# Kernel tuning notes

Measured on AMD Instinct MI355X. Metric: run time of the kernel, lower is better.

The kernel has to match this reference:

```python
import jax, jax.numpy as jnp
import numpy as np

N = 100000   # nodes
E = 1600000  # random edges per augmented graph (before self-loops)
F = 128      # input_dim
H = 128      # hidden_dim
K = 3        # n_clusters
L = 3        # num_layers


def setup_inputs() -> dict:
    key = jax.random.key(0)
    ks = jax.random.split(key, 24)
    x1 = jax.random.normal(ks[0], (N, F), jnp.float32)
    x2 = jax.random.normal(ks[1], (N, F), jnp.float32)
    x3 = jax.random.normal(ks[2], (N, F), jnp.float32)
    loops = jnp.arange(N, dtype=jnp.int32)
    self_loops = jnp.stack([loops, loops])  # [2, N]

    def aug_edges(k):
        e = jax.random.randint(k, (2, E), 0, N, dtype=jnp.int32)
        return jnp.concatenate([e, self_loops], axis=1)  # [2, E+N]

    e1 = aug_edges(ks[3])
    e2 = aug_edges(ks[4])
    e3 = aug_edges(ks[5])

    s = 1.0 / np.sqrt(H)
    Ws = jax.random.normal(ks[6], (L, H, H), jnp.float32) * s  # F == H
    bs = jnp.zeros((L, H), jnp.float32)
    a = jnp.float32(0.25)  # PReLU slope (torch default)
    cw1 = jax.random.normal(ks[7], (H, H), jnp.float32) * s
    cb1 = jnp.zeros((H,), jnp.float32)
    cw2 = jax.random.normal(ks[8], (H, K), jnp.float32) * s
    cb2 = jnp.zeros((K,), jnp.float32)
    iw1 = jax.random.normal(ks[9], (H, H), jnp.float32) * s
    ib1 = jnp.zeros((H,), jnp.float32)
    iw2 = jax.random.normal(ks[10], (H, H), jnp.float32) * s
    ib2 = jnp.zeros((H,), jnp.float32)
    return dict(x1=x1, x2=x2, x3=x3, e1=e1, e2=e2, e3=e3,
                Ws=Ws, bs=bs, a=a, cw1=cw1, cb1=cb1, cw2=cw2, cb2=cb2,
                iw1=iw1, ib1=ib1, iw2=iw2, ib2=ib2)


def _l2norm(z):
    # F.normalize(z, dim=1), eps=1e-12
    return z / jnp.maximum(jnp.linalg.norm(z, axis=1, keepdims=True), 1e-12)


def _gconv(x, edges, Ws, bs, a):
    # DGL GraphConv norm='left': messages from src scaled by 1/out_deg(src),
    # summed at dst, then linear + shared PReLU per layer; final row L2-norm.
    src, dst = edges[0], edges[1]
    deg = jax.ops.segment_sum(jnp.ones(src.shape[0], x.dtype), src, num_segments=N)
    inv = 1.0 / jnp.maximum(deg, 1.0)  # DGL clamps zero out-degree
    z = x
    for l in range(L):
        msg = (z * inv[:, None])[src]               # [E, H] gather
        agg = jax.ops.segment_sum(msg, dst, num_segments=N)  # [N, H] scatter-add
        z = agg @ Ws[l] + bs[l]
        z = jnp.where(z >= 0, z, a * z)             # PReLU
    return _l2norm(z)


def reference(x1, x2, x3, e1, e2, e3, Ws, bs, a,
              cw1, cb1, cw2, cb2, iw1, ib1, iw2, ib2):
    z1 = _gconv(x1, e1, Ws, bs, a)
    z2 = _gconv(x2, e2, Ws, bs, a)
    z3 = _gconv(x3, e3, Ws, bs, a)

    def cluster(z):
        h = jax.nn.elu(z @ cw1 + cb1)
        p = jax.nn.softmax(h @ cw2 + cb2, axis=1)
        return _l2norm(p)

    def inst(z):
        return jax.nn.elu(z @ iw1 + ib1) @ iw2 + ib2

    return (z3, inst(z1), inst(z2), cluster(z1), cluster(z2))
```

## Files before the change

kernel.cpp:

```cpp
#include <hip/hip_runtime.h>
#include <hip/hip_bf16.h>
#include <cmath>


typedef __attribute__((ext_vector_type(8))) short short8;
typedef __attribute__((ext_vector_type(4))) float floatx4;

#define NB_MAX 512
#define PART_B 256
#define LCSR_MAX 6144

static __device__ __forceinline__ unsigned short f2bf(float f) {
  unsigned u = __builtin_bit_cast(unsigned, f);
  u += 0x7fffu + ((u >> 16) & 1u);
  return (unsigned short)(u >> 16);
}
static __device__ __forceinline__ float bf2f(unsigned short h) {
  unsigned u = ((unsigned)h) << 16;
  return __builtin_bit_cast(float, u);
}
static __device__ __forceinline__ float bflo(unsigned v) {
  return __builtin_bit_cast(float, v << 16);
}
static __device__ __forceinline__ float bfhi(unsigned v) {
  return __builtin_bit_cast(float, v & 0xffff0000u);
}

static __device__ __forceinline__ floatx4 mfma16(short8 a, short8 b, floatx4 c) {
  return __builtin_amdgcn_mfma_f32_16x16x32_bf16(a, b, c, 0, 0, 0);
}

static __device__ __forceinline__ void mfma_block(
    const short8 a_h[2], const unsigned short* __restrict__ Wth,
    const unsigned short* __restrict__ Wtl, int ks, int lr, int lg,
    floatx4 acc[2][8]) {
#pragma unroll
  for (int nf = 0; nf < 8; ++nf) {
    size_t boff = (size_t)(nf * 16 + lr) * 128 + ks * 32 + lg * 8;
    short8 b_h = *(const short8*)(Wth + boff);
    short8 b_l = *(const short8*)(Wtl + boff);
#pragma unroll
    for (int mf = 0; mf < 2; ++mf) {
      acc[mf][nf] = mfma16(a_h[mf], b_h, acc[mf][nf]);
      acc[mf][nf] = mfma16(a_h[mf], b_l, acc[mf][nf]);
    }
  }
}


__global__ __launch_bounds__(256) void bucket_count(const int* __restrict__ src,
                                                    const int* __restrict__ dst,
                                                    int ne, int nb, int chunk,
                                                    int* __restrict__ bcnt,
                                                    int* __restrict__ deg) {
  __shared__ int h[NB_MAX];
  const int t = threadIdx.x, b = blockIdx.x;
  for (int i = t; i < nb; i += 256) h[i] = 0;
  __syncthreads();
  const int start = b * chunk, endi = min(start + chunk, ne);
  for (int i = start + t; i < endi; i += 256) {
    atomicAdd(&h[dst[i] >> 8], 1);
    atomicAdd(&deg[src[i]], 1);
  }
  __syncthreads();
  for (int i = t; i < nb; i += 256) bcnt[i * PART_B + b] = h[i];
}

__global__ __launch_bounds__(256) void partition_edges(
    const int* __restrict__ src, const int* __restrict__ dst, int ne, int nb,
    int chunk, const int* __restrict__ boff, int* __restrict__ part) {
  __shared__ int h[NB_MAX];
  const int t = threadIdx.x, b = blockIdx.x;
  for (int i = t; i < nb; i += 256) h[i] = boff[i * PART_B + b];
  __syncthreads();
  const int start = b * chunk, endi = min(start + chunk, ne);
  for (int i = start + t; i < endi; i += 256) {
    int d = dst[i];
    int gpos = atomicAdd(&h[d >> 8], 1);
    part[gpos] = (src[i] << 8) | (d & 255);
  }
}

__global__ __launch_bounds__(256) void fine_csr(const int* __restrict__ part,
                                                const int* __restrict__ boff,
                                                int nb, int n, int ne,
                                                int* __restrict__ row_ptr,
                                                int* __restrict__ csr) {
  __shared__ int s[256];
  __shared__ int cur[256];
  __shared__ int lcsr[LCSR_MAX];
  const int t = threadIdx.x, b2 = blockIdx.x;
  const int base = boff[b2 * PART_B];
  const int endb = boff[(b2 + 1) * PART_B];
  const int cnt_local = endb - base;
  const int node_base = b2 << 8;

  s[t] = 0;
  __syncthreads();
  for (int i = base + t; i < endb; i += 256) atomicAdd(&s[part[i] & 255], 1);
  __syncthreads();
  for (int d = 1; d < 256; d <<= 1) {
    int v = s[t];
    int a = (t >= d) ? s[t - d] : 0;
    __syncthreads();
    s[t] = v + a;
    __syncthreads();
  }
  int excl = (t == 0) ? 0 : s[t - 1];
  int node = node_base + t;
  if (node <= n) row_ptr[node] = base + excl;
  if (b2 == nb - 1 && t == 0) row_ptr[n] = ne;
  cur[t] = excl;
  __syncthreads();

  if (cnt_local <= LCSR_MAX) {
    for (int i = base + t; i < endb; i += 256) {
      int v = part[i];
      int p = atomicAdd(&cur[v & 255], 1);
      lcsr[p] = v >> 8;
    }
    __syncthreads();
    for (int i = t; i < cnt_local; i += 256) csr[base + i] = lcsr[i];
  } else {
    for (int i = base + t; i < endb; i += 256) {
      int v = part[i];
      int p = atomicAdd(&cur[v & 255], 1);
      csr[base + p] = v >> 8;
    }
  }
}

__global__ __launch_bounds__(256) void make_inv(const int* __restrict__ deg,
                                                float* __restrict__ inv, int n) {
  int i = blockIdx.x * blockDim.x + threadIdx.x;
  if (i < n) inv[i] = 1.0f / (float)(deg[i] + 1);
}

#define SCAN_B 256
#define SCAN_T 256

__global__ __launch_bounds__(SCAN_T) void scan_part(const int* __restrict__ cnt,
                                                    int n, int cpt,
                                                    int* __restrict__ partials) {
  __shared__ int red[SCAN_T];
  const int t = threadIdx.x, b = blockIdx.x;
  const int g = b * SCAN_T + t;
  const int start = g * cpt, endi = min(start + cpt, n);
  int s = 0;
  for (int i = start; i < endi; ++i) s += cnt[i];
  red[t] = s;
  __syncthreads();
  for (int d = SCAN_T / 2; d > 0; d >>= 1) {
    if (t < d) red[t] += red[t + d];
    __syncthreads();
  }
  if (t == 0) partials[b] = red[0];
}

__global__ __launch_bounds__(SCAN_B) void scan_offsets(
    const int* __restrict__ partials, int* __restrict__ block_off,
    int* __restrict__ row_ptr, int n) {
  __shared__ int sums[SCAN_B];
  const int t = threadIdx.x;
  sums[t] = partials[t];
  __syncthreads();
  for (int d = 1; d < SCAN_B; d <<= 1) {
    int v = sums[t];
    int a = (t >= d) ? sums[t - d] : 0;
    __syncthreads();
    sums[t] = v + a;
    __syncthreads();
  }
  block_off[t] = (t == 0) ? 0 : sums[t - 1];
  if (t == SCAN_B - 1) row_ptr[n] = sums[t];
}

__global__ __launch_bounds__(SCAN_T) void scan_fill(const int* __restrict__ cnt,
                                                    int n, int cpt,
                                                    const int* __restrict__ block_off,
                                                    int* __restrict__ row_ptr) {
  __shared__ int sums[SCAN_T];
  const int t = threadIdx.x, b = blockIdx.x;
  const int g = b * SCAN_T + t;
  const int start = g * cpt, endi = min(start + cpt, n);
  int s = 0;
  for (int i = start; i < endi; ++i) s += cnt[i];
  sums[t] = s;
  __syncthreads();
  for (int d = 1; d < SCAN_T; d <<= 1) {
    int v = sums[t];
    int a = (t >= d) ? sums[t - d] : 0;
    __syncthreads();
    sums[t] = v + a;
    __syncthreads();
  }
  int off = block_off[b] + ((t == 0) ? 0 : sums[t - 1]);
  for (int i = start; i < endi; ++i) {
    row_ptr[i] = off;
    off += cnt[i];
  }
}


__global__ __launch_bounds__(256) void scale_cast(const float* __restrict__ x,
                                                  const float* __restrict__ inv,
                                                  unsigned short* __restrict__ zsc,
                                                  int n) {
  int idx = blockIdx.x * blockDim.x + threadIdx.x;
  if (idx >= n * 32) return;
  int row = idx >> 5;
  float s = inv[row];
  float4 v = *(const float4*)(x + (size_t)idx * 4);
  unsigned u0 = (unsigned)f2bf(v.x * s) | ((unsigned)f2bf(v.y * s) << 16);
  unsigned u1 = (unsigned)f2bf(v.z * s) | ((unsigned)f2bf(v.w * s) << 16);
  uint2 p = {u0, u1};
  *(uint2*)(zsc + (size_t)idx * 4) = p;
}

__global__ __launch_bounds__(256) void prep_w(const float* __restrict__ src,
                                              unsigned short* __restrict__ dh,
                                              unsigned short* __restrict__ dl) {
  int idx = blockIdx.x * 256 + threadIdx.x;
  int k = idx >> 7, nn = idx & 127;
  float w = src[idx];
  unsigned short h = f2bf(w);
  dh[nn * 128 + k] = h;
  dl[nn * 128 + k] = f2bf(w - bf2f(h));
}


__global__ __launch_bounds__(256) void aggregate_bf16(
    const unsigned short* __restrict__ zsc, const int* __restrict__ row_ptr,
    const int* __restrict__ csr_src, unsigned short* __restrict__ ah, int n) {
  int w = (blockIdx.x * blockDim.x + threadIdx.x) >> 6;
  const int lane = threadIdx.x & 63;
  if (w >= n) return;
  w = __builtin_amdgcn_readfirstlane(w);
  const int beg = row_ptr[w], end = row_ptr[w + 1];
  const unsigned* zp = (const unsigned*)zsc;
  unsigned vs = zp[(size_t)w * 64 + lane];
  float ax0 = bflo(vs), ay0 = bfhi(vs), ax1 = 0.f, ay1 = 0.f;
  float ax2 = 0.f, ay2 = 0.f, ax3 = 0.f, ay3 = 0.f;
  for (int base = beg; base < end; base += 64) {
    const int cnt = min(64, end - base);
    int my = (base + lane < end) ? csr_src[base + lane] : 0;
    int e = 0;
    for (; e + 8 <= cnt; e += 8) {
      int s0 = __shfl(my, e);
      int s1 = __shfl(my, e + 1);
      int s2 = __shfl(my, e + 2);
      int s3 = __shfl(my, e + 3);
      int s4 = __shfl(my, e + 4);
      int s5 = __shfl(my, e + 5);
      int s6 = __shfl(my, e + 6);
      int s7 = __shfl(my, e + 7);
      unsigned v0 = zp[(size_t)s0 * 64 + lane];
      unsigned v1 = zp[(size_t)s1 * 64 + lane];
      unsigned v2 = zp[(size_t)s2 * 64 + lane];
      unsigned v3 = zp[(size_t)s3 * 64 + lane];
      unsigned v4 = zp[(size_t)s4 * 64 + lane];
      unsigned v5 = zp[(size_t)s5 * 64 + lane];
      unsigned v6 = zp[(size_t)s6 * 64 + lane];
      unsigned v7 = zp[(size_t)s7 * 64 + lane];
      ax0 += bflo(v0); ay0 += bfhi(v0);
      ax1 += bflo(v1); ay1 += bfhi(v1);
      ax2 += bflo(v2); ay2 += bfhi(v2);
      ax3 += bflo(v3); ay3 += bfhi(v3);
      ax0 += bflo(v4); ay0 += bfhi(v4);
      ax1 += bflo(v5); ay1 += bfhi(v5);
      ax2 += bflo(v6); ay2 += bfhi(v6);
      ax3 += bflo(v7); ay3 += bfhi(v7);
    }
    for (; e + 4 <= cnt; e += 4) {
      int s0 = __shfl(my, e);
      int s1 = __shfl(my, e + 1);
      int s2 = __shfl(my, e + 2);
      int s3 = __shfl(my, e + 3);
      unsigned v0 = zp[(size_t)s0 * 64 + lane];
      unsigned v1 = zp[(size_t)s1 * 64 + lane];
      unsigned v2 = zp[(size_t)s2 * 64 + lane];
      unsigned v3 = zp[(size_t)s3 * 64 + lane];
      ax0 += bflo(v0); ay0 += bfhi(v0);
      ax1 += bflo(v1); ay1 += bfhi(v1);
      ax2 += bflo(v2); ay2 += bfhi(v2);
      ax3 += bflo(v3); ay3 += bfhi(v3);
    }
    for (; e < cnt; ++e) {
      int s0 = __shfl(my, e);
      unsigned v0 = zp[(size_t)s0 * 64 + lane];
      ax0 += bflo(v0);
      ay0 += bfhi(v0);
    }
  }
  float ax = (ax0 + ax1) + (ax2 + ax3);
  float ay = (ay0 + ay1) + (ay2 + ay3);
  ((unsigned*)ah)[(size_t)w * 64 + lane] =
      (unsigned)f2bf(ax) | ((unsigned)f2bf(ay) << 16);
}

template <int MODE>
__global__ __launch_bounds__(256) void gemm_one(
    const unsigned short* __restrict__ Ah,
    const unsigned short* __restrict__ Wth, const unsigned short* __restrict__ Wtl,
    const float* __restrict__ bias, float* __restrict__ outf,
    unsigned short* __restrict__ o_h, const float* __restrict__ inv,
    const float* __restrict__ slope_ptr, int n) {
  const int tid = threadIdx.x;
  const int wave = tid >> 6, lane = tid & 63;
  const int lr = lane & 15;
  const int lg = lane >> 4;
  const int m0 = blockIdx.x * 128 + wave * 32;

  floatx4 acc[2][8];
#pragma unroll
  for (int mf = 0; mf < 2; ++mf)
#pragma unroll
    for (int nf = 0; nf < 8; ++nf) acc[mf][nf] = (floatx4){0.f, 0.f, 0.f, 0.f};

#pragma unroll
  for (int ks = 0; ks < 4; ++ks) {
    short8 a_h[2];
#pragma unroll
    for (int mf = 0; mf < 2; ++mf) {
      size_t aoff = (size_t)(m0 + mf * 16 + lr) * 128 + ks * 32 + lg * 8;
      a_h[mf] = *(const short8*)(Ah + aoff);
    }
    mfma_block(a_h, Wth, Wtl, ks, lr, lg, acc);
  }

  float bv[8];
#pragma unroll
  for (int nf = 0; nf < 8; ++nf) bv[nf] = bias[nf * 16 + lr];
  const float slope = *slope_ptr;

#pragma unroll
  for (int mf = 0; mf < 2; ++mf) {
#pragma unroll
    for (int reg = 0; reg < 4; ++reg) {
      const int row = m0 + mf * 16 + lg * 4 + reg;
      float v[8];
#pragma unroll
      for (int nf = 0; nf < 8; ++nf) {
        float t = acc[mf][nf][reg] + bv[nf];
        v[nf] = (t >= 0.f) ? t : t * slope;
      }
      if constexpr (MODE == 0) {
        float s = inv[row < n ? row : 0];
#pragma unroll
        for (int nf = 0; nf < 8; ++nf)
          o_h[(size_t)row * 128 + nf * 16 + lr] = f2bf(v[nf] * s);
      } else {
        float ss = 0.f;
#pragma unroll
        for (int nf = 0; nf < 8; ++nf) ss = fmaf(v[nf], v[nf], ss);
        ss += __shfl_xor(ss, 1);
        ss += __shfl_xor(ss, 2);
        ss += __shfl_xor(ss, 4);
        ss += __shfl_xor(ss, 8);
        float r = 1.f / fmaxf(sqrtf(ss), 1e-12f);
        if (row < n) {
#pragma unroll
          for (int nf = 0; nf < 8; ++nf)
            outf[(size_t)row * 128 + nf * 16 + lr] = v[nf] * r;
        }
      }
    }
  }
}

__global__ __launch_bounds__(256) void head_fused(
    const unsigned short* __restrict__ Ah,
    const unsigned short* __restrict__ W3h, const unsigned short* __restrict__ W3l,
    const float* __restrict__ b3,
    const unsigned short* __restrict__ IW1h, const unsigned short* __restrict__ IW1l,
    const float* __restrict__ ib1,
    const unsigned short* __restrict__ IW2h, const unsigned short* __restrict__ IW2l,
    const float* __restrict__ ib2,
    const unsigned short* __restrict__ CW1h, const unsigned short* __restrict__ CW1l,
    const float* __restrict__ cb1,
    const float* __restrict__ cw2, const float* __restrict__ cb2,
    const float* __restrict__ slope_ptr,
    float* __restrict__ out_inst, float* __restrict__ out_clu, int n) {
  __shared__ unsigned short zl[128][132];
  const int tid = threadIdx.x;
  const int wave = tid >> 6, lane = tid & 63;
  const int lr = lane & 15, lg = lane >> 4;
  const int mw = wave * 32;
  const int m0g = blockIdx.x * 128 + mw;
  const float slope = *slope_ptr;

  floatx4 acc[2][8];

#pragma unroll
  for (int mf = 0; mf < 2; ++mf)
#pragma unroll
    for (int nf = 0; nf < 8; ++nf) acc[mf][nf] = (floatx4){0.f, 0.f, 0.f, 0.f};
#pragma unroll
  for (int ks = 0; ks < 4; ++ks) {
    short8 a_h[2];
#pragma unroll
    for (int mf = 0; mf < 2; ++mf) {
      size_t aoff = (size_t)(m0g + mf * 16 + lr) * 128 + ks * 32 + lg * 8;
      a_h[mf] = *(const short8*)(Ah + aoff);
    }
    mfma_block(a_h, W3h, W3l, ks, lr, lg, acc);
  }
  {
    float bv[8];
#pragma unroll
    for (int nf = 0; nf < 8; ++nf) bv[nf] = b3[nf * 16 + lr];
#pragma unroll
    for (int mf = 0; mf < 2; ++mf) {
#pragma unroll
      for (int reg = 0; reg < 4; ++reg) {
        const int lrow = mw + mf * 16 + lg * 4 + reg;
        float v[8];
#pragma unroll
        for (int nf = 0; nf < 8; ++nf) {
          float t = acc[mf][nf][reg] + bv[nf];
          v[nf] = (t >= 0.f) ? t : t * slope;
        }
        float ss = 0.f;
#pragma unroll
        for (int nf = 0; nf < 8; ++nf) ss = fmaf(v[nf], v[nf], ss);
        ss += __shfl_xor(ss, 1);
        ss += __shfl_xor(ss, 2);
        ss += __shfl_xor(ss, 4);
        ss += __shfl_xor(ss, 8);
        float r = 1.f / fmaxf(sqrtf(ss), 1e-12f);
#pragma unroll
        for (int nf = 0; nf < 8; ++nf)
          zl[lrow][nf * 16 + lr] = f2bf(v[nf] * r);
      }
    }
  }
  __syncthreads();

#pragma unroll
  for (int mf = 0; mf < 2; ++mf)
#pragma unroll
    for (int nf = 0; nf < 8; ++nf) acc[mf][nf] = (floatx4){0.f, 0.f, 0.f, 0.f};
#pragma unroll
  for (int ks = 0; ks < 4; ++ks) {
    short8 a_h[2];
#pragma unroll
    for (int mf = 0; mf < 2; ++mf)
      a_h[mf] = *(const short8*)(&zl[mw + mf * 16 + lr][ks * 32 + lg * 8]);
    mfma_block(a_h, CW1h, CW1l, ks, lr, lg, acc);
  }
  {
    float bv[8], c2v[8][3];
#pragma unroll
    for (int nf = 0; nf < 8; ++nf) {
      bv[nf] = cb1[nf * 16 + lr];
      int col = nf * 16 + lr;
#pragma unroll
      for (int c = 0; c < 3; ++c) c2v[nf][c] = cw2[col * 3 + c];
    }
#pragma unroll
    for (int mf = 0; mf < 2; ++mf) {
#pragma unroll
      for (int reg = 0; reg < 4; ++reg) {
        const int row = m0g + mf * 16 + lg * 4 + reg;
        float p[3] = {0.f, 0.f, 0.f};
#pragma unroll
        for (int nf = 0; nf < 8; ++nf) {
          float t = acc[mf][nf][reg] + bv[nf];
          t = (t > 0.f) ? t : expm1f(t);
#pragma unroll
          for (int c = 0; c < 3; ++c) p[c] = fmaf(t, c2v[nf][c], p[c]);
        }
#pragma unroll
        for (int c = 0; c < 3; ++c) {
          p[c] += __shfl_xor(p[c], 1);
          p[c] += __shfl_xor(p[c], 2);
          p[c] += __shfl_xor(p[c], 4);
          p[c] += __shfl_xor(p[c], 8);
          p[c] += cb2[c];
        }
        float mx = fmaxf(p[0], fmaxf(p[1], p[2]));
        float e0 = expf(p[0] - mx), e1 = expf(p[1] - mx), e2 = expf(p[2] - mx);
        float sden = e0 + e1 + e2;
        float q0 = e0 / sden, q1 = e1 / sden, q2 = e2 / sden;
        float nr =
            1.f / fmaxf(sqrtf(fmaf(q0, q0, fmaf(q1, q1, q2 * q2))), 1e-12f);
        if (row < n && lr < 3) {
          float val = (lr == 0) ? q0 * nr : (lr == 1) ? q1 * nr : q2 * nr;
          out_clu[(size_t)row * 3 + lr] = val;
        }
      }
    }
  }
  __syncthreads();

#pragma unroll
  for (int mf = 0; mf < 2; ++mf)
#pragma unroll
    for (int nf = 0; nf < 8; ++nf) acc[mf][nf] = (floatx4){0.f, 0.f, 0.f, 0.f};
#pragma unroll
  for (int ks = 0; ks < 4; ++ks) {
    short8 a_h[2];
#pragma unroll
    for (int mf = 0; mf < 2; ++mf)
      a_h[mf] = *(const short8*)(&zl[mw + mf * 16 + lr][ks * 32 + lg * 8]);
    mfma_block(a_h, IW1h, IW1l, ks, lr, lg, acc);
  }
  {
    float bv[8];
#pragma unroll
    for (int nf = 0; nf < 8; ++nf) bv[nf] = ib1[nf * 16 + lr];
#pragma unroll
    for (int mf = 0; mf < 2; ++mf) {
#pragma unroll
      for (int reg = 0; reg < 4; ++reg) {
        const int lrow = mw + mf * 16 + lg * 4 + reg;
#pragma unroll
        for (int nf = 0; nf < 8; ++nf) {
          float t = acc[mf][nf][reg] + bv[nf];
          t = (t > 0.f) ? t : expm1f(t);
          zl[lrow][nf * 16 + lr] = f2bf(t);
        }
      }
    }
  }
  __syncthreads();

#pragma unroll
  for (int mf = 0; mf < 2; ++mf)
#pragma unroll
    for (int nf = 0; nf < 8; ++nf) acc[mf][nf] = (floatx4){0.f, 0.f, 0.f, 0.f};
#pragma unroll
  for (int ks = 0; ks < 4; ++ks) {
    short8 a_h[2];
#pragma unroll
    for (int mf = 0; mf < 2; ++mf)
      a_h[mf] = *(const short8*)(&zl[mw + mf * 16 + lr][ks * 32 + lg * 8]);
    mfma_block(a_h, IW2h, IW2l, ks, lr, lg, acc);
  }
  {
    float bv[8];
#pragma unroll
    for (int nf = 0; nf < 8; ++nf) bv[nf] = ib2[nf * 16 + lr];
#pragma unroll
    for (int mf = 0; mf < 2; ++mf) {
#pragma unroll
      for (int reg = 0; reg < 4; ++reg) {
        const int row = m0g + mf * 16 + lg * 4 + reg;
        if (row < n) {
#pragma unroll
          for (int nf = 0; nf < 8; ++nf)
            out_inst[(size_t)row * 128 + nf * 16 + lr] =
                acc[mf][nf][reg] + bv[nf];
        }
      }
    }
  }
}


extern "C" void kernel_launch(void* const* d_in, const int* in_sizes, int n_in,
                              void* d_out, int out_size, void* d_ws,
                              size_t ws_size, hipStream_t stream) {
  const int H = 128;
  const int N = in_sizes[0] / H;
  const int Npad = (N + 127) & ~127;
  const int NB = (N + 255) >> 8;

  char* ws = (char*)d_ws;
  size_t off = 0;
  auto take = [&](size_t bytes) -> void* {
    void* p = ws + off;
    off = (off + bytes + 255) & ~(size_t)255;
    return p;
  };
  float* inv = (float*)take((size_t)N * 4);
  int* deg = (int*)take((size_t)N * 4);
  int* row_ptr = (int*)take((size_t)(N + 1) * 4);
  int* bcnt = (int*)take((size_t)NB * PART_B * 4);
  int* boff = (int*)take(((size_t)NB * PART_B + 1) * 4);
  int* partials = (int*)take((size_t)SCAN_B * 4);
  int* block_off = (int*)take((size_t)SCAN_B * 4);
  int ne_max = 0;
  for (int g = 0; g < 3; ++g) ne_max = max(ne_max, in_sizes[3 + g] / 2);
  int* csr = (int*)take((size_t)ne_max * 4);
  int* part = (int*)take((size_t)ne_max * 4);
  unsigned short* wth = (unsigned short*)take((size_t)6 * 16384 * 2);
  unsigned short* wtl = (unsigned short*)take((size_t)6 * 16384 * 2);
  unsigned short* ah = (unsigned short*)take((size_t)Npad * 128 * 2);
  unsigned short* zsc = (unsigned short*)take((size_t)Npad * 128 * 2);

  const float* Ws = (const float*)d_in[6];
  const float* bs = (const float*)d_in[7];
  const float* a_ptr = (const float*)d_in[8];
  const float* cw1 = (const float*)d_in[9];
  const float* cb1 = (const float*)d_in[10];
  const float* cw2 = (const float*)d_in[11];
  const float* cb2 = (const float*)d_in[12];
  const float* iw1 = (const float*)d_in[13];
  const float* ib1 = (const float*)d_in[14];
  const float* iw2 = (const float*)d_in[15];
  const float* ib2 = (const float*)d_in[16];

  float* outp = (float*)d_out;
  float* out_z3 = outp;
  float* out_inst[2] = {outp + (size_t)N * H, outp + 2 * (size_t)N * H};
  float* out_clu[2] = {outp + 3 * (size_t)N * H,
                       outp + 3 * (size_t)N * H + (size_t)N * 3};

  const float* wsrc[6] = {Ws, Ws + 16384, Ws + 2 * 16384, iw1, iw2, cw1};
  for (int m = 0; m < 6; ++m)
    prep_w<<<64, 256, 0, stream>>>(wsrc[m], wth + m * 16384, wtl + m * 16384);

  const int aggBlocks = (N + 3) / 4;
  const int gemmBlocks = Npad / 128;
  const int nscan = NB * PART_B;
  const int cpt = (nscan + SCAN_B * SCAN_T - 1) / (SCAN_B * SCAN_T);

  for (int g = 0; g < 3; ++g) {
    const float* x = (const float*)d_in[g];
    const int* edges = (const int*)d_in[3 + g];
    const int ne = in_sizes[3 + g] / 2;
    const int neR = (ne > N) ? (ne - N) : 0;
    const int* src = edges;
    const int* dst = edges + ne;
    const int chunk = (neR + PART_B - 1) / PART_B;

    hipMemsetAsync(deg, 0, (size_t)N * 4, stream);
    bucket_count<<<PART_B, 256, 0, stream>>>(src, dst, neR, NB, chunk, bcnt,
                                             deg);
    make_inv<<<(N + 255) / 256, 256, 0, stream>>>(deg, inv, N);
    scan_part<<<SCAN_B, SCAN_T, 0, stream>>>(bcnt, nscan, cpt, partials);
    scan_offsets<<<1, SCAN_B, 0, stream>>>(partials, block_off, boff, nscan);
    scan_fill<<<SCAN_B, SCAN_T, 0, stream>>>(bcnt, nscan, cpt, block_off, boff);
    partition_edges<<<PART_B, 256, 0, stream>>>(src, dst, neR, NB, chunk, boff,
                                                part);
    fine_csr<<<NB, 256, 0, stream>>>(part, boff, NB, N, neR, row_ptr, csr);

    scale_cast<<<(N * 32 + 255) / 256, 256, 0, stream>>>(x, inv, zsc, N);

    for (int l = 0; l < 2; ++l) {
      aggregate_bf16<<<aggBlocks, 256, 0, stream>>>(zsc, row_ptr, csr, ah, N);
      gemm_one<0><<<gemmBlocks, 256, 0, stream>>>(
          ah, wth + l * 16384, wtl + l * 16384, bs + l * 128, nullptr, zsc, inv,
          a_ptr, N);
    }
    aggregate_bf16<<<aggBlocks, 256, 0, stream>>>(zsc, row_ptr, csr, ah, N);
    if (g == 2) {
      gemm_one<1><<<gemmBlocks, 256, 0, stream>>>(
          ah, wth + 2 * 16384, wtl + 2 * 16384, bs + 2 * 128, out_z3, nullptr,
          nullptr, a_ptr, N);
    } else {
      head_fused<<<gemmBlocks, 256, 0, stream>>>(
          ah, wth + 2 * 16384, wtl + 2 * 16384, bs + 2 * 128,
          wth + 3 * 16384, wtl + 3 * 16384, ib1,
          wth + 4 * 16384, wtl + 4 * 16384, ib2,
          wth + 5 * 16384, wtl + 5 * 16384, cb1,
          cw2, cb2, a_ptr, out_inst[g], out_clu[g], N);
    }
  }
}
```

Before: 1.519 ms.

## Store features in column-sliced layout and aggregate one 32-byte slice per block

Node features move from row-major bf16 into 8 column slices of 16 features each, laid out slice-major, so each aggregation block works on one slice. A single 2 MB-per-slice working set can then stay cache-resident while neighbors are gathered at random. Each wave handles 16 rows and gathers 8 edges at once, with 8 lanes covering one 32-byte slice row, then reduces across lanes with shuffles. The GEMM A-loads and the layer-output writes are rewritten to match the new layout. In exchange, each gather is only 32 bytes, the CSR indices are read 8 times, and the GEMM loads become strided.

```diff
diff --git a/kernel.cpp b/kernel.cpp
--- a/kernel.cpp
+++ b/kernel.cpp
@@ -9,6 +9,7 @@
 #define NB_MAX 512
 #define PART_B 256
 #define LCSR_MAX 6144
+#define AGG_RPW 16
 
 static __device__ __forceinline__ unsigned short f2bf(float f) {
   unsigned u = __builtin_bit_cast(unsigned, f);
@@ -45,6 +46,13 @@
       acc[mf][nf] = mfma16(a_h[mf], b_l, acc[mf][nf]);
     }
   }
+}
+
+static __device__ __forceinline__ short8 a_frag(
+    const unsigned short* __restrict__ A, int npad, int row, int ks, int lg) {
+  const int col0 = ks * 32 + lg * 8;
+  return *(const short8*)(A + ((size_t)(col0 >> 4) * npad + row) * 16 +
+                          (col0 & 15));
 }
 
 
@@ -204,17 +212,19 @@
 
 __global__ __launch_bounds__(256) void scale_cast(const float* __restrict__ x,
                                                   const float* __restrict__ inv,
-                                                  unsigned short* __restrict__ zsc,
-                                                  int n) {
+                                                  unsigned* __restrict__ zs,
+                                                  int n, int npad) {
   int idx = blockIdx.x * blockDim.x + threadIdx.x;
   if (idx >= n * 32) return;
-  int row = idx >> 5;
+  int row = idx >> 5, q = idx & 31;
   float s = inv[row];
   float4 v = *(const float4*)(x + (size_t)idx * 4);
   unsigned u0 = (unsigned)f2bf(v.x * s) | ((unsigned)f2bf(v.y * s) << 16);
   unsigned u1 = (unsigned)f2bf(v.z * s) | ((unsigned)f2bf(v.w * s) << 16);
-  uint2 p = {u0, u1};
-  *(uint2*)(zsc + (size_t)idx * 4) = p;
+  int slice = q >> 2;
+  int co = (q & 3) << 1;
+  uint2 pk = {u0, u1};
+  *(uint2*)(zs + ((size_t)slice * npad + row) * 8 + co) = pk;
 }
 
 __global__ __launch_bounds__(256) void prep_w(const float* __restrict__ src,
@@ -229,73 +239,76 @@
 }
 
 
-__global__ __launch_bounds__(256) void aggregate_bf16(
-    const unsigned short* __restrict__ zsc, const int* __restrict__ row_ptr,
-    const int* __restrict__ csr_src, unsigned short* __restrict__ ah, int n) {
-  int w = (blockIdx.x * blockDim.x + threadIdx.x) >> 6;
+__global__ __launch_bounds__(256) void aggregate_slice2(
+    const unsigned* __restrict__ zs, const int* __restrict__ row_ptr,
+    const int* __restrict__ csr_src, unsigned* __restrict__ ah, int n,
+    int npad) {
   const int lane = threadIdx.x & 63;
-  if (w >= n) return;
-  w = __builtin_amdgcn_readfirstlane(w);
-  const int beg = row_ptr[w], end = row_ptr[w + 1];
-  const unsigned* zp = (const unsigned*)zsc;
-  unsigned vs = zp[(size_t)w * 64 + lane];
-  float ax0 = bflo(vs), ay0 = bfhi(vs), ax1 = 0.f, ay1 = 0.f;
-  float ax2 = 0.f, ay2 = 0.f, ax3 = 0.f, ay3 = 0.f;
-  for (int base = beg; base < end; base += 64) {
-    const int cnt = min(64, end - base);
-    int my = (base + lane < end) ? csr_src[base + lane] : 0;
-    int e = 0;
-    for (; e + 8 <= cnt; e += 8) {
-      int s0 = __shfl(my, e);
-      int s1 = __shfl(my, e + 1);
-      int s2 = __shfl(my, e + 2);
-      int s3 = __shfl(my, e + 3);
-      int s4 = __shfl(my, e + 4);
-      int s5 = __shfl(my, e + 5);
-      int s6 = __shfl(my, e + 6);
-      int s7 = __shfl(my, e + 7);
-      unsigned v0 = zp[(size_t)s0 * 64 + lane];
-      unsigned v1 = zp[(size_t)s1 * 64 + lane];
-      unsigned v2 = zp[(size_t)s2 * 64 + lane];
-      unsigned v3 = zp[(size_t)s3 * 64 + lane];
-      unsigned v4 = zp[(size_t)s4 * 64 + lane];
-      unsigned v5 = zp[(size_t)s5 * 64 + lane];
-      unsigned v6 = zp[(size_t)s6 * 64 + lane];
-      unsigned v7 = zp[(size_t)s7 * 64 + lane];
-      ax0 += bflo(v0); ay0 += bfhi(v0);
-      ax1 += bflo(v1); ay1 += bfhi(v1);
-      ax2 += bflo(v2); ay2 += bfhi(v2);
-      ax3 += bflo(v3); ay3 += bfhi(v3);
-      ax0 += bflo(v4); ay0 += bfhi(v4);
-      ax1 += bflo(v5); ay1 += bfhi(v5);
-      ax2 += bflo(v6); ay2 += bfhi(v6);
-      ax3 += bflo(v7); ay3 += bfhi(v7);
-    }
-    for (; e + 4 <= cnt; e += 4) {
-      int s0 = __shfl(my, e);
-      int s1 = __shfl(my, e + 1);
-      int s2 = __shfl(my, e + 2);
-      int s3 = __shfl(my, e + 3);
-      unsigned v0 = zp[(size_t)s0 * 64 + lane];
-      unsigned v1 = zp[(size_t)s1 * 64 + lane];
-      unsigned v2 = zp[(size_t)s2 * 64 + lane];
-      unsigned v3 = zp[(size_t)s3 * 64 + lane];
-      ax0 += bflo(v0); ay0 += bfhi(v0);
-      ax1 += bflo(v1); ay1 += bfhi(v1);
-      ax2 += bflo(v2); ay2 += bfhi(v2);
-      ax3 += bflo(v3); ay3 += bfhi(v3);
-    }
-    for (; e < cnt; ++e) {
-      int s0 = __shfl(my, e);
-      unsigned v0 = zp[(size_t)s0 * 64 + lane];
-      ax0 += bflo(v0);
-      ay0 += bfhi(v0);
-    }
-  }
-  float ax = (ax0 + ax1) + (ax2 + ax3);
-  float ay = (ay0 + ay1) + (ay2 + ay3);
-  ((unsigned*)ah)[(size_t)w * 64 + lane] =
-      (unsigned)f2bf(ax) | ((unsigned)f2bf(ay) << 16);
+  const int wid = threadIdx.x >> 6;
+  const int slice = blockIdx.x & 7;
+  const int rblk = blockIdx.x >> 3;
+  const int g = lane >> 3;
+  const int c = lane & 7;
+  const unsigned* zb = zs + (size_t)slice * npad * 8;
+  unsigned* ab = ah + (size_t)slice * npad * 8;
+  const int r0 = (rblk * 4 + wid) * AGG_RPW;
+  if (r0 >= n) return;
+
+  for (int rr = 0; rr < AGG_RPW; ++rr) {
+    const int r = r0 + rr;
+    if (r >= n) return;
+    const int beg = row_ptr[r], end = row_ptr[r + 1];
+    const unsigned vself = zb[(size_t)r * 8 + c];
+    float axA = 0.f, ayA = 0.f, axB = 0.f, ayB = 0.f;
+    for (int base = beg; base < end; base += 64) {
+      const int chunk = min(64, end - base);
+      int my = (base + lane < end)
+                   ? __builtin_nontemporal_load(csr_src + base + lane)
+                   : 0;
+      int e = 0;
+      for (; e + 32 <= chunk; e += 32) {
+        int sA = __shfl(my, e + g);
+        int sB = __shfl(my, e + 8 + g);
+        int sC = __shfl(my, e + 16 + g);
+        int sD = __shfl(my, e + 24 + g);
+        unsigned vA = zb[(size_t)sA * 8 + c];
+        unsigned vB = zb[(size_t)sB * 8 + c];
+        unsigned vC = zb[(size_t)sC * 8 + c];
+        unsigned vD = zb[(size_t)sD * 8 + c];
+        axA += bflo(vA); ayA += bfhi(vA);
+        axB += bflo(vB); ayB += bfhi(vB);
+        axA += bflo(vC); ayA += bfhi(vC);
+        axB += bflo(vD); ayB += bfhi(vD);
+      }
+      for (; e + 8 <= chunk; e += 8) {
+        int s0 = __shfl(my, e + g);
+        unsigned v0 = zb[(size_t)s0 * 8 + c];
+        axA += bflo(v0);
+        ayA += bfhi(v0);
+      }
+      if (e < chunk) {
+        int s0 = __shfl(my, min(e + g, chunk - 1));
+        unsigned v0 = zb[(size_t)s0 * 8 + c];
+        float m = (g < chunk - e) ? 1.f : 0.f;
+        axA = fmaf(m, bflo(v0), axA);
+        ayA = fmaf(m, bfhi(v0), ayA);
+      }
+    }
+    float ax = axA + axB, ay = ayA + ayB;
+    ax += __shfl_xor(ax, 8);
+    ay += __shfl_xor(ay, 8);
+    ax += __shfl_xor(ax, 16);
+    ay += __shfl_xor(ay, 16);
+    ax += __shfl_xor(ax, 32);
+    ay += __shfl_xor(ay, 32);
+    if (lane < 8) {
+      ax += bflo(vself);
+      ay += bfhi(vself);
+      __builtin_nontemporal_store(
+          (unsigned)f2bf(ax) | ((unsigned)f2bf(ay) << 16),
+          ab + (size_t)r * 8 + lane);
+    }
+  }
 }
 
 template <int MODE>
@@ -304,7 +317,7 @@
     const unsigned short* __restrict__ Wth, const unsigned short* __restrict__ Wtl,
     const float* __restrict__ bias, float* __restrict__ outf,
     unsigned short* __restrict__ o_h, const float* __restrict__ inv,
-    const float* __restrict__ slope_ptr, int n) {
+    const float* __restrict__ slope_ptr, int n, int npad) {
   const int tid = threadIdx.x;
   const int wave = tid >> 6, lane = tid & 63;
   const int lr = lane & 15;
@@ -321,10 +334,8 @@
   for (int ks = 0; ks < 4; ++ks) {
     short8 a_h[2];
 #pragma unroll
-    for (int mf = 0; mf < 2; ++mf) {
-      size_t aoff = (size_t)(m0 + mf * 16 + lr) * 128 + ks * 32 + lg * 8;
-      a_h[mf] = *(const short8*)(Ah + aoff);
-    }
+    for (int mf = 0; mf < 2; ++mf)
+      a_h[mf] = a_frag(Ah, npad, m0 + mf * 16 + lr, ks, lg);
     mfma_block(a_h, Wth, Wtl, ks, lr, lg, acc);
   }
 
@@ -348,7 +359,7 @@
         float s = inv[row < n ? row : 0];
 #pragma unroll
         for (int nf = 0; nf < 8; ++nf)
-          o_h[(size_t)row * 128 + nf * 16 + lr] = f2bf(v[nf] * s);
+          o_h[((size_t)nf * npad + row) * 16 + lr] = f2bf(v[nf] * s);
       } else {
         float ss = 0.f;
 #pragma unroll
@@ -380,7 +391,8 @@
     const float* __restrict__ cb1,
     const float* __restrict__ cw2, const float* __restrict__ cb2,
     const float* __restrict__ slope_ptr,
-    float* __restrict__ out_inst, float* __restrict__ out_clu, int n) {
+    float* __restrict__ out_inst, float* __restrict__ out_clu, int n,
+    int npad) {
   __shared__ unsigned short zl[128][132];
   const int tid = threadIdx.x;
   const int wave = tid >> 6, lane = tid & 63;
@@ -399,10 +411,8 @@
   for (int ks = 0; ks < 4; ++ks) {
     short8 a_h[2];
 #pragma unroll
-    for (int mf = 0; mf < 2; ++mf) {
-      size_t aoff = (size_t)(m0g + mf * 16 + lr) * 128 + ks * 32 + lg * 8;
-      a_h[mf] = *(const short8*)(Ah + aoff);
-    }
+    for (int mf = 0; mf < 2; ++mf)
+      a_h[mf] = a_frag(Ah, npad, m0g + mf * 16 + lr, ks, lg);
     mfma_block(a_h, W3h, W3l, ks, lr, lg, acc);
   }
   {
@@ -611,7 +621,7 @@
   for (int m = 0; m < 6; ++m)
     prep_w<<<64, 256, 0, stream>>>(wsrc[m], wth + m * 16384, wtl + m * 16384);
 
-  const int aggBlocks = (N + 3) / 4;
+  const int aggBlocks = 8 * ((N + 4 * AGG_RPW - 1) / (4 * AGG_RPW));
   const int gemmBlocks = Npad / 128;
   const int nscan = NB * PART_B;
   const int cpt = (nscan + SCAN_B * SCAN_T - 1) / (SCAN_B * SCAN_T);
@@ -636,26 +646,30 @@
                                                 part);
     fine_csr<<<NB, 256, 0, stream>>>(part, boff, NB, N, neR, row_ptr, csr);
 
-    scale_cast<<<(N * 32 + 255) / 256, 256, 0, stream>>>(x, inv, zsc, N);
+    scale_cast<<<(N * 32 + 255) / 256, 256, 0, stream>>>(x, inv,
+                                                         (unsigned*)zsc, N,
+                                                         Npad);
 
     for (int l = 0; l < 2; ++l) {
-      aggregate_bf16<<<aggBlocks, 256, 0, stream>>>(zsc, row_ptr, csr, ah, N);
+      aggregate_slice2<<<aggBlocks, 256, 0, stream>>>(
+          (const unsigned*)zsc, row_ptr, csr, (unsigned*)ah, N, Npad);
       gemm_one<0><<<gemmBlocks, 256, 0, stream>>>(
           ah, wth + l * 16384, wtl + l * 16384, bs + l * 128, nullptr, zsc, inv,
-          a_ptr, N);
-    }
-    aggregate_bf16<<<aggBlocks, 256, 0, stream>>>(zsc, row_ptr, csr, ah, N);
+          a_ptr, N, Npad);
+    }
+    aggregate_slice2<<<aggBlocks, 256, 0, stream>>>(
+        (const unsigned*)zsc, row_ptr, csr, (unsigned*)ah, N, Npad);
     if (g == 2) {
       gemm_one<1><<<gemmBlocks, 256, 0, stream>>>(
           ah, wth + 2 * 16384, wtl + 2 * 16384, bs + 2 * 128, out_z3, nullptr,
-          nullptr, a_ptr, N);
+          nullptr, a_ptr, N, Npad);
     } else {
       head_fused<<<gemmBlocks, 256, 0, stream>>>(
           ah, wth + 2 * 16384, wtl + 2 * 16384, bs + 2 * 128,
           wth + 3 * 16384, wtl + 3 * 16384, ib1,
           wth + 4 * 16384, wtl + 4 * 16384, ib2,
           wth + 5 * 16384, wtl + 5 * 16384, cb1,
-          cw2, cb2, a_ptr, out_inst[g], out_clu[g], N);
-    }
-  }
-}
+          cw2, cb2, a_ptr, out_inst[g], out_clu[g], N, Npad);
+    }
+  }
+}
```

After: 3.215 ms. 112% more time.
